# Kernel optimization log

Measured on AMD Instinct MI355X. Metric: run time of the kernel, lower is better.

## Reference

```python
import jax, jax.numpy as jnp
import numpy as np

B, C, H, W = 64, 8, 256, 256
OUT_C, K = 8, 3
IN_FEAT = 8  # Linear in_channels


def setup_inputs() -> dict:
    key = jax.random.key(0)
    k1, k2, k3, k4 = jax.random.split(key, 4)
    x = jax.random.normal(k1, (B, C, H, W), dtype=jnp.float32)
    dynamic_weights = jax.random.normal(k2, (B, C, IN_FEAT), dtype=jnp.float32)
    # kernel_generator: Linear(in_channels -> out_channels*k*k)
    lim = 1.0 / np.sqrt(IN_FEAT)
    Wg = jax.random.uniform(k3, (OUT_C * K * K, IN_FEAT), dtype=jnp.float32, minval=-lim, maxval=lim)
    bg = jax.random.uniform(k4, (OUT_C * K * K,), dtype=jnp.float32, minval=-lim, maxval=lim)
    return {"x": x, "dynamic_weights": dynamic_weights, "Wg": Wg, "bg": bg}


def reference(x, dynamic_weights, Wg, bg):
    b, c, h, w = x.shape
    # per-sample kernel generation: (B, C, in_feat) @ (in_feat, OUT_C*K*K)
    lin = jnp.einsum('bci,oi->bco', dynamic_weights, Wg) + bg  # (B, C, OUT_C*K*K)
    # torch .view(B, out_C, C, k, k) reinterprets the row-major buffer
    kernels = lin.reshape(b, OUT_C, c, K, K)
    # batch-as-groups grouped conv: input (1, B*C, H, W), kernel (B*OUT_C, C, K, K)
    x1 = x.reshape(1, b * c, h, w)
    kern = kernels.reshape(b * OUT_C, c, K, K)
    out = jax.lax.conv_general_dilated(
        x1, kern,
        window_strides=(1, 1),
        padding=((1, 1), (1, 1)),
        dimension_numbers=('NCHW', 'OIHW', 'NCHW'),
        feature_group_count=b,
    )
    return out.reshape(b, OUT_C, h, w)
```

## Files before the change

kernel.cpp:

```cpp
#include <hip/hip_runtime.h>


#define HC   65536
#define WW   256
#define RPB  4

typedef float floatx2 __attribute__((ext_vector_type(2)));

__global__ __launch_bounds__(576) void gen_kernels(
    const float* __restrict__ dw,
    const float* __restrict__ Wg,
    const float* __restrict__ bg,
    float* __restrict__ kern)
{
    const int b = blockIdx.x;
    const int j = threadIdx.x;
    if (j >= 576) return;
    const int ic   = j / 72;
    const int rem  = j % 72;
    const int kh   = rem / 24;
    const int rem2 = rem % 24;
    const int kw   = rem2 / 8;
    const int oc   = rem2 % 8;
    const int o    = ic * 9 + kh * 3 + kw;

    const float* d = dw + b * 64 + oc * 8;
    const float* g = Wg + o * 8;
    float v = bg[o];
#pragma unroll
    for (int i = 0; i < 8; ++i) v = fmaf(d[i], g[i], v);
    kern[b * 576 + j] = v;
}

__global__ __launch_bounds__(256) void dyn_conv_pk(
    const float* __restrict__ x,
    const float* __restrict__ kern,
    float* __restrict__ out)
{
    const int b  = blockIdx.y;
    const int h0 = blockIdx.x * RPB;
    const int w  = threadIdx.x;

    const float*   xb  = x + (size_t)b * 8 * HC;
    const floatx2* Kb2 = reinterpret_cast<const floatx2*>(kern + b * 576);
    float*         ob  = out + (size_t)b * 8 * HC;

    floatx2 acc[RPB][4];
#pragma unroll
    for (int r = 0; r < RPB; ++r)
#pragma unroll
        for (int p = 0; p < 4; ++p) acc[r][p] = (floatx2)(0.f);

#pragma unroll 1
    for (int ic = 0; ic < 8; ++ic) {
        floatx2 wk2[36];
        const floatx2* Kic2 = Kb2 + ic * 36;
#pragma unroll
        for (int t = 0; t < 36; ++t) wk2[t] = Kic2[t];

        const float* xch = xb + ic * HC;
#pragma unroll
        for (int ri = 0; ri < RPB + 2; ++ri) {
            const int row = h0 - 1 + ri;
            float xm = 0.f, xc = 0.f, xp = 0.f;
            if (row >= 0 && row < 256) {
                const float* xr = xch + row * WW;
                xc = xr[w];
                xm = (w > 0)   ? xr[w - 1] : 0.f;
                xp = (w < 255) ? xr[w + 1] : 0.f;
            }
            const floatx2 vm = {xm, xm};
            const floatx2 vc = {xc, xc};
            const floatx2 vp = {xp, xp};
#pragma unroll
            for (int kh = 0; kh < 3; ++kh) {
                const int ro = ri - kh;
                if (ro < 0 || ro >= RPB) continue;
                const floatx2* wr = &wk2[kh * 12];
#pragma unroll
                for (int p = 0; p < 4; ++p) {
                    floatx2 a = acc[ro][p];
                    a = __builtin_elementwise_fma(vm, wr[0 * 4 + p], a);
                    a = __builtin_elementwise_fma(vc, wr[1 * 4 + p], a);
                    a = __builtin_elementwise_fma(vp, wr[2 * 4 + p], a);
                    acc[ro][p] = a;
                }
            }
        }
    }

    const int hw0 = h0 * WW + w;
#pragma unroll
    for (int p = 0; p < 4; ++p) {
        float* orow0 = ob + (2 * p)     * HC + hw0;
        float* orow1 = ob + (2 * p + 1) * HC + hw0;
#pragma unroll
        for (int r = 0; r < RPB; ++r) {
            orow0[r * WW] = acc[r][p].x;
            orow1[r * WW] = acc[r][p].y;
        }
    }
}

__global__ __launch_bounds__(256) void dyn_conv_fused(
    const float* __restrict__ x,
    const float* __restrict__ dw,
    const float* __restrict__ Wg,
    const float* __restrict__ bg,
    float* __restrict__ out)
{
    __shared__ float kl[576];
    const int b  = blockIdx.y;
    const int h0 = blockIdx.x * RPB;
    const int w  = threadIdx.x;

    for (int j = threadIdx.x; j < 576; j += 256) {
        const int ic   = j / 72;
        const int rem  = j % 72;
        const int kh   = rem / 24;
        const int rem2 = rem % 24;
        const int kw   = rem2 / 8;
        const int oc   = rem2 % 8;
        const int o    = ic * 9 + kh * 3 + kw;
        const float* d = dw + b * 64 + oc * 8;
        const float* g = Wg + o * 8;
        float v = bg[o];
#pragma unroll
        for (int i = 0; i < 8; ++i) v = fmaf(d[i], g[i], v);
        kl[j] = v;
    }
    __syncthreads();

    const float* xb = x + (size_t)b * 8 * HC;
    float*       ob = out + (size_t)b * 8 * HC;

    float acc[RPB][8];
#pragma unroll
    for (int r = 0; r < RPB; ++r)
#pragma unroll
        for (int oc = 0; oc < 8; ++oc) acc[r][oc] = 0.f;

#pragma unroll 1
    for (int ic = 0; ic < 8; ++ic) {
        const float* xch = xb + ic * HC;
#pragma unroll
        for (int ri = 0; ri < RPB + 2; ++ri) {
            const int row = h0 - 1 + ri;
            float xm = 0.f, xc = 0.f, xp = 0.f;
            if (row >= 0 && row < 256) {
                const float* xr = xch + row * WW;
                xc = xr[w];
                xm = (w > 0)   ? xr[w - 1] : 0.f;
                xp = (w < 255) ? xr[w + 1] : 0.f;
            }
#pragma unroll
            for (int kh = 0; kh < 3; ++kh) {
                const int ro = ri - kh;
                if (ro < 0 || ro >= RPB) continue;
                const float* wr = &kl[0] + ic * 72 + kh * 24;
#pragma unroll
                for (int oc = 0; oc < 8; ++oc) {
                    float a = acc[ro][oc];
                    a = fmaf(xm, wr[0 * 8 + oc], a);
                    a = fmaf(xc, wr[1 * 8 + oc], a);
                    a = fmaf(xp, wr[2 * 8 + oc], a);
                    acc[ro][oc] = a;
                }
            }
        }
    }

    const int hw0 = h0 * WW + w;
#pragma unroll
    for (int oc = 0; oc < 8; ++oc) {
        float* orow = ob + oc * HC + hw0;
#pragma unroll
        for (int r = 0; r < RPB; ++r) orow[r * WW] = acc[r][oc];
    }
}

extern "C" void kernel_launch(void* const* d_in, const int* in_sizes, int n_in,
                              void* d_out, int out_size, void* d_ws, size_t ws_size,
                              hipStream_t stream) {
    const float* x  = (const float*)d_in[0];
    const float* dw = (const float*)d_in[1];
    const float* Wg = (const float*)d_in[2];
    const float* bg = (const float*)d_in[3];
    float* out = (float*)d_out;

    const dim3 grid(256 / RPB, 64);
    const dim3 block(256);

    if (ws_size >= (size_t)(64 * 576 * sizeof(float))) {
        float* kern = (float*)d_ws;
        gen_kernels<<<dim3(64), dim3(576), 0, stream>>>(dw, Wg, bg, kern);
        dyn_conv_pk<<<grid, block, 0, stream>>>(x, kern, out);
    } else {
        dyn_conv_fused<<<grid, block, 0, stream>>>(x, dw, Wg, bg, out);
    }
}
```

Before: 242.3 us.

## Remap conv threads to one row per wave with four columns per lane

Each thread now computes 4 adjacent columns of a single output row instead of 4 rows of one column. A wave handles a row, so inputs load as float4 plus two halo scalars and outputs store as float4. This trades vertical reuse across rows (6 row reads for 4 outputs) for horizontal reuse (3 row reads per output row, with vector width 4). The goal is fewer load and store instructions, with more input rows reloaded per output in exchange.

```diff
diff --git a/kernel.cpp b/kernel.cpp
--- a/kernel.cpp
+++ b/kernel.cpp
@@ -6,6 +6,7 @@
 #define RPB  4
 
 typedef float floatx2 __attribute__((ext_vector_type(2)));
+typedef float floatx4 __attribute__((ext_vector_type(4)));
 
 __global__ __launch_bounds__(576) void gen_kernels(
     const float* __restrict__ dw,
@@ -32,24 +33,26 @@
     kern[b * 576 + j] = v;
 }
 
-__global__ __launch_bounds__(256) void dyn_conv_pk(
+__global__ __launch_bounds__(256) void dyn_conv_v4c(
     const float* __restrict__ x,
     const float* __restrict__ kern,
     float* __restrict__ out)
 {
-    const int b  = blockIdx.y;
-    const int h0 = blockIdx.x * RPB;
-    const int w  = threadIdx.x;
+    const int b    = blockIdx.y;
+    const int wv   = threadIdx.x >> 6;
+    const int lane = threadIdx.x & 63;
+    const int h    = blockIdx.x * RPB + wv;
+    const int w4   = lane << 2;
 
     const float*   xb  = x + (size_t)b * 8 * HC;
     const floatx2* Kb2 = reinterpret_cast<const floatx2*>(kern + b * 576);
     float*         ob  = out + (size_t)b * 8 * HC;
 
-    floatx2 acc[RPB][4];
-#pragma unroll
-    for (int r = 0; r < RPB; ++r)
-#pragma unroll
-        for (int p = 0; p < 4; ++p) acc[r][p] = (floatx2)(0.f);
+    floatx2 acc[4][4];
+#pragma unroll
+    for (int c = 0; c < 4; ++c)
+#pragma unroll
+        for (int p = 0; p < 4; ++p) acc[c][p] = (floatx2)(0.f);
 
 #pragma unroll 1
     for (int ic = 0; ic < 8; ++ic) {
@@ -60,45 +63,44 @@
 
         const float* xch = xb + ic * HC;
 #pragma unroll
-        for (int ri = 0; ri < RPB + 2; ++ri) {
-            const int row = h0 - 1 + ri;
-            float xm = 0.f, xc = 0.f, xp = 0.f;
+        for (int kh = 0; kh < 3; ++kh) {
+            const int row = h - 1 + kh;
+            float xs[6];
+#pragma unroll
+            for (int t = 0; t < 6; ++t) xs[t] = 0.f;
             if (row >= 0 && row < 256) {
-                const float* xr = xch + row * WW;
-                xc = xr[w];
-                xm = (w > 0)   ? xr[w - 1] : 0.f;
-                xp = (w < 255) ? xr[w + 1] : 0.f;
-            }
-            const floatx2 vm = {xm, xm};
-            const floatx2 vc = {xc, xc};
-            const floatx2 vp = {xp, xp};
-#pragma unroll
-            for (int kh = 0; kh < 3; ++kh) {
-                const int ro = ri - kh;
-                if (ro < 0 || ro >= RPB) continue;
-                const floatx2* wr = &wk2[kh * 12];
+                const float* xrow = xch + row * WW;
+                const floatx4 v = *reinterpret_cast<const floatx4*>(xrow + w4);
+                xs[1] = v.x; xs[2] = v.y; xs[3] = v.z; xs[4] = v.w;
+                xs[0] = (w4 > 0)      ? xrow[w4 - 1] : 0.f;
+                xs[5] = (w4 + 4 < WW) ? xrow[w4 + 4] : 0.f;
+            }
+            const floatx2* wr = &wk2[kh * 12];
+#pragma unroll
+            for (int c = 0; c < 4; ++c) {
+                const floatx2 t0 = {xs[c],     xs[c]};
+                const floatx2 t1 = {xs[c + 1], xs[c + 1]};
+                const floatx2 t2 = {xs[c + 2], xs[c + 2]};
 #pragma unroll
                 for (int p = 0; p < 4; ++p) {
-                    floatx2 a = acc[ro][p];
-                    a = __builtin_elementwise_fma(vm, wr[0 * 4 + p], a);
-                    a = __builtin_elementwise_fma(vc, wr[1 * 4 + p], a);
-                    a = __builtin_elementwise_fma(vp, wr[2 * 4 + p], a);
-                    acc[ro][p] = a;
+                    floatx2 a = acc[c][p];
+                    a = __builtin_elementwise_fma(t0, wr[0 * 4 + p], a);
+                    a = __builtin_elementwise_fma(t1, wr[1 * 4 + p], a);
+                    a = __builtin_elementwise_fma(t2, wr[2 * 4 + p], a);
+                    acc[c][p] = a;
                 }
             }
         }
     }
 
-    const int hw0 = h0 * WW + w;
+    const size_t o0 = (size_t)h * WW + w4;
 #pragma unroll
     for (int p = 0; p < 4; ++p) {
-        float* orow0 = ob + (2 * p)     * HC + hw0;
-        float* orow1 = ob + (2 * p + 1) * HC + hw0;
-#pragma unroll
-        for (int r = 0; r < RPB; ++r) {
-            orow0[r * WW] = acc[r][p].x;
-            orow1[r * WW] = acc[r][p].y;
-        }
+        floatx4 v0, v1;
+        v0.x = acc[0][p].x; v0.y = acc[1][p].x; v0.z = acc[2][p].x; v0.w = acc[3][p].x;
+        v1.x = acc[0][p].y; v1.y = acc[1][p].y; v1.z = acc[2][p].y; v1.w = acc[3][p].y;
+        *reinterpret_cast<floatx4*>(ob + (2 * p)     * HC + o0) = v0;
+        *reinterpret_cast<floatx4*>(ob + (2 * p + 1) * HC + o0) = v1;
     }
 }
 
@@ -194,7 +196,7 @@
     if (ws_size >= (size_t)(64 * 576 * sizeof(float))) {
         float* kern = (float*)d_ws;
         gen_kernels<<<dim3(64), dim3(576), 0, stream>>>(dw, Wg, bg, kern);
-        dyn_conv_pk<<<grid, block, 0, stream>>>(x, kern, out);
+        dyn_conv_v4c<<<grid, block, 0, stream>>>(x, kern, out);
     } else {
         dyn_conv_fused<<<grid, block, 0, stream>>>(x, dw, Wg, bg, out);
     }
```

New measurement: 258.0 us. +6.5%, slower.

## Stage input halo rows into LDS via direct global-to-LDS loads

Applied to the files above, without the earlier changes.

The conv kernel now copies all 8 input channels' 6 halo rows (48KB) into shared memory up front, using the async global_load_lds builtin with 16-byte transfers, then reads the three horizontal taps from LDS. Previously each thread issued three global loads per row per channel. This cuts redundant global and L1 traffic and issues all loads before compute, at the cost of 48KB LDS per block, which limits occupancy, and one barrier with no overlap between loading and compute.

```diff
diff --git a/kernel.cpp b/kernel.cpp
--- a/kernel.cpp
+++ b/kernel.cpp
@@ -6,6 +6,12 @@
 #define RPB  4
 
 typedef float floatx2 __attribute__((ext_vector_type(2)));
+
+__device__ __forceinline__ void gload_lds16(const float* g, float* l) {
+    __builtin_amdgcn_global_load_lds(
+        (const __attribute__((address_space(1))) void*)g,
+        (__attribute__((address_space(3))) void*)l, 16, 0, 0);
+}
 
 __global__ __launch_bounds__(576) void gen_kernels(
     const float* __restrict__ dw,
@@ -32,18 +38,47 @@
     kern[b * 576 + j] = v;
 }
 
-__global__ __launch_bounds__(256) void dyn_conv_pk(
+__global__ __launch_bounds__(256) void dyn_conv_lds(
     const float* __restrict__ x,
     const float* __restrict__ kern,
     float* __restrict__ out)
 {
-    const int b  = blockIdx.y;
-    const int h0 = blockIdx.x * RPB;
-    const int w  = threadIdx.x;
+    __shared__ float sx[8][6][256];
+
+    const int b    = blockIdx.y;
+    const int h0   = blockIdx.x * RPB;
+    const int w    = threadIdx.x;
+    const int wv   = threadIdx.x >> 6;
+    const int lane = threadIdx.x & 63;
 
     const float*   xb  = x + (size_t)b * 8 * HC;
     const floatx2* Kb2 = reinterpret_cast<const floatx2*>(kern + b * 576);
     float*         ob  = out + (size_t)b * 8 * HC;
+
+    if (h0 == 0) {
+#pragma unroll
+        for (int ic = 0; ic < 8; ++ic) sx[ic][0][w] = 0.f;
+    }
+    if (h0 == 256 - RPB) {
+#pragma unroll
+        for (int ic = 0; ic < 8; ++ic) sx[ic][5][w] = 0.f;
+    }
+
+#pragma unroll
+    for (int ic = 0; ic < 8; ++ic) {
+        const float* xch = xb + ic * HC;
+#pragma unroll
+        for (int r0 = 0; r0 < 2; ++r0) {
+            const int r = wv + r0 * 4;
+            if (r < 6) {
+                const int row = h0 - 1 + r;
+                if (row >= 0 && row < 256) {
+                    gload_lds16(xch + row * WW + (lane << 2), &sx[ic][r][0]);
+                }
+            }
+        }
+    }
+    __syncthreads();
 
     floatx2 acc[RPB][4];
 #pragma unroll
@@ -58,17 +93,11 @@
 #pragma unroll
         for (int t = 0; t < 36; ++t) wk2[t] = Kic2[t];
 
-        const float* xch = xb + ic * HC;
 #pragma unroll
         for (int ri = 0; ri < RPB + 2; ++ri) {
-            const int row = h0 - 1 + ri;
-            float xm = 0.f, xc = 0.f, xp = 0.f;
-            if (row >= 0 && row < 256) {
-                const float* xr = xch + row * WW;
-                xc = xr[w];
-                xm = (w > 0)   ? xr[w - 1] : 0.f;
-                xp = (w < 255) ? xr[w + 1] : 0.f;
-            }
+            const float xc = sx[ic][ri][w];
+            const float xm = (w > 0)   ? sx[ic][ri][w - 1] : 0.f;
+            const float xp = (w < 255) ? sx[ic][ri][w + 1] : 0.f;
             const floatx2 vm = {xm, xm};
             const floatx2 vc = {xc, xc};
             const floatx2 vp = {xp, xp};
@@ -194,7 +223,7 @@
     if (ws_size >= (size_t)(64 * 576 * sizeof(float))) {
         float* kern = (float*)d_ws;
         gen_kernels<<<dim3(64), dim3(576), 0, stream>>>(dw, Wg, bg, kern);
-        dyn_conv_pk<<<grid, block, 0, stream>>>(x, kern, out);
+        dyn_conv_lds<<<grid, block, 0, stream>>>(x, kern, out);
     } else {
         dyn_conv_fused<<<grid, block, 0, stream>>>(x, dw, Wg, bg, out);
     }
```

After: 241.8 us. Within noise of the previous version (-0.2%).
